# Performance work log

Hardware: AMD Instinct MI355X
Metric: run time of the kernel (lower is better)

Reference implementation:

```python
import jax, jax.numpy as jnp
import numpy as np

B, S, DIN, DOUT = 4, 4096, 4096, 4096
W_SCALE = 0.02  # kaiming-ish scale; keeps values inside fp8 range


def setup_inputs() -> dict:
    key = jax.random.key(0)
    k1, k2, k3 = jax.random.split(key, 3)
    x = jax.random.normal(k1, (B, S, DIN), dtype=jnp.float16)
    weight = (jax.random.normal(k2, (DOUT, DIN), dtype=jnp.float32) * W_SCALE).astype(jnp.float16)
    bias = (jax.random.normal(k3, (DOUT,), dtype=jnp.float32) * W_SCALE).astype(jnp.float16)
    return {"x": x, "weight": weight, "bias": bias}


def reference(x, weight, bias):
    # Emulate torch._scaled_mm: activations quantized to fp8 e5m2,
    # weight (transposed) quantized to fp8 e4m3fn, scale_a = scale_b = 1.0,
    # accumulate in fp32, add fp16 bias, output fp16.
    out_shape = x.shape[:-1] + (weight.shape[0],)
    x8 = x.reshape(-1, x.shape[-1]).astype(jnp.float8_e5m2)       # [M, DIN]
    w8 = weight.T.astype(jnp.float8_e4m3fn)                        # [DIN, DOUT]
    scale = jnp.float32(1.0)  # scale_a * scale_b
    acc = jnp.matmul(x8.astype(jnp.float32), w8.astype(jnp.float32))  # [M, DOUT] fp32 accum
    out = (acc * scale + bias.astype(jnp.float32)).astype(jnp.float16)
    return out.reshape(out_shape)
```

## Files before the change

### kernel.cpp

```cpp
#include <hip/hip_runtime.h>
#include <hip/hip_fp16.h>

#define M_DIM 16384
#define N_DIM 4096
#define K_DIM 4096

typedef __attribute__((ext_vector_type(16))) float f32x16;
typedef __attribute__((ext_vector_type(4)))  int   i32x4;
typedef __attribute__((ext_vector_type(8)))  int   i32x8;

union frag_u { i32x8 v; i32x4 h[2]; };

template<bool E4M3>
__global__ __launch_bounds__(256) void quant_tile_kernel(
    const float* __restrict__ in,
    uint4* __restrict__ out,
    int ngrp)
{
  int t = blockIdx.x * 256 + threadIdx.x;
  if (t >= ngrp) return;
  const int g    = t & 1023;
  const int tile = t >> 10;
  const int kt   = tile & 63;
  const int bt   = tile >> 6;
  const int sb   = g >> 7;
  const int half = (g >> 6) & 1;
  const int l    = g & 63;
  const int row  = bt * 256 + sb * 32 + (l & 31);
  const int k    = kt * 64 + (l >> 5) * 32 + half * 16;

  const float4* p = reinterpret_cast<const float4*>(in + (size_t)row * K_DIM + k);
  float4 v0 = p[0], v1 = p[1], v2 = p[2], v3 = p[3];
  int w0 = 0, w1 = 0, w2 = 0, w3 = 0;
  if (E4M3) {
    w0 = __builtin_amdgcn_cvt_pk_fp8_f32(v0.x, v0.y, w0, false);
    w0 = __builtin_amdgcn_cvt_pk_fp8_f32(v0.z, v0.w, w0, true);
    w1 = __builtin_amdgcn_cvt_pk_fp8_f32(v1.x, v1.y, w1, false);
    w1 = __builtin_amdgcn_cvt_pk_fp8_f32(v1.z, v1.w, w1, true);
    w2 = __builtin_amdgcn_cvt_pk_fp8_f32(v2.x, v2.y, w2, false);
    w2 = __builtin_amdgcn_cvt_pk_fp8_f32(v2.z, v2.w, w2, true);
    w3 = __builtin_amdgcn_cvt_pk_fp8_f32(v3.x, v3.y, w3, false);
    w3 = __builtin_amdgcn_cvt_pk_fp8_f32(v3.z, v3.w, w3, true);
  } else {
    w0 = __builtin_amdgcn_cvt_pk_bf8_f32(v0.x, v0.y, w0, false);
    w0 = __builtin_amdgcn_cvt_pk_bf8_f32(v0.z, v0.w, w0, true);
    w1 = __builtin_amdgcn_cvt_pk_bf8_f32(v1.x, v1.y, w1, false);
    w1 = __builtin_amdgcn_cvt_pk_bf8_f32(v1.z, v1.w, w1, true);
    w2 = __builtin_amdgcn_cvt_pk_bf8_f32(v2.x, v2.y, w2, false);
    w2 = __builtin_amdgcn_cvt_pk_bf8_f32(v2.z, v2.w, w2, true);
    w3 = __builtin_amdgcn_cvt_pk_bf8_f32(v3.x, v3.y, w3, false);
    w3 = __builtin_amdgcn_cvt_pk_bf8_f32(v3.z, v3.w, w3, true);
  }
  out[t] = make_uint4((unsigned)w0, (unsigned)w1, (unsigned)w2, (unsigned)w3);
}

__global__ __launch_bounds__(512, 2) void gemm_fp8_kernel(
    const unsigned char* __restrict__ Aq,
    const unsigned char* __restrict__ Wq,
    const float* __restrict__ bias,
    float* __restrict__ C)
{
  __shared__ __align__(16) unsigned char lds[131072];

  const int tid  = threadIdx.x;
  const int lane = tid & 63;
  const int wave = tid >> 6;
  const int wr   = wave >> 2;
  const int wc   = wave & 3;

  const int bid = blockIdx.x;
  const int swz = (bid & 7) * 128 + (bid >> 3);
  const int bmi = swz >> 4;
  const int bni = swz & 15;

  const unsigned char* tA = Aq + (size_t)bmi * (64 * 16384);
  const unsigned char* tB = Wq + (size_t)bni * (64 * 16384);

  const size_t t16 = (size_t)tid * 16;
  const int    w1k = wave * 1024;

#define STAGE(gb, lo_)                                                      \
  __builtin_amdgcn_global_load_lds(                                        \
      (const __attribute__((address_space(1))) void*)((gb) + t16),          \
      (__attribute__((address_space(3))) void*)(lds + (lo_) + w1k), 16, 0, 0)

#define STAGE_TILE(tp, base)                                                \
  STAGE(tA + (tp), (base));          STAGE(tA + (tp) + 8192, (base) + 8192); \
  STAGE(tB + (tp), (base) + 16384);  STAGE(tB + (tp) + 8192, (base) + 24576)

#define RD8(dst, off)                                                       \
  { const unsigned char* _p = lds + (off) + lane * 16;                      \
    (dst).h[0] = *reinterpret_cast<const i32x4*>(_p);                       \
    (dst).h[1] = *reinterpret_cast<const i32x4*>(_p + 1024); }

#define MFMA(d, a, b)                                                       \
  d = __builtin_amdgcn_mfma_scale_f32_32x32x64_f8f6f4(                      \
      a, b, d, 1 , 0 , 0, 0x7F7F7F7F, 0, 0x7F7F7F7F)

#define SBAR __builtin_amdgcn_sched_barrier(0)
#define P1   __builtin_amdgcn_s_setprio(1)
#define P0   __builtin_amdgcn_s_setprio(0)

  const int aoff = wr * 8192;
  const int boff = 16384 + wc * 4096;

  f32x16 acc[4][2] = {};
  frag_u Ea0, Ea1, Ea2, Ea3, Eb0, Eb1;
  frag_u Oa0, Oa1, Oa2, Oa3, Ob0, Ob1;

#define RDTILE(s, buf)                                                      \
  RD8(s##a0, (buf) + aoff);        RD8(s##a1, (buf) + aoff + 2048);         \
  RD8(s##a2, (buf) + aoff + 4096); RD8(s##a3, (buf) + aoff + 6144);         \
  RD8(s##b0, (buf) + boff);        RD8(s##b1, (buf) + boff + 2048)

#define TILE_STEP(rdset, mfset, rdbuf, stbuf, tp3)                          \
  SBAR;                                                                     \
  RDTILE(rdset, rdbuf);                                                     \
  SBAR;                                                                     \
  P1;                                                                       \
  MFMA(acc[0][0], mfset##a0.v, mfset##b0.v);                                \
  MFMA(acc[0][1], mfset##a0.v, mfset##b1.v);                                \
  MFMA(acc[1][0], mfset##a1.v, mfset##b0.v);                                \
  MFMA(acc[1][1], mfset##a1.v, mfset##b1.v);                                \
  MFMA(acc[2][0], mfset##a2.v, mfset##b0.v);                                \
  MFMA(acc[2][1], mfset##a2.v, mfset##b1.v);                                \
  MFMA(acc[3][0], mfset##a3.v, mfset##b0.v);                                \
  MFMA(acc[3][1], mfset##a3.v, mfset##b1.v);                                \
  P0;                                                                       \
  SBAR;                                                                     \
  STAGE_TILE(tp3, stbuf);                                                   \
  SBAR;                                                                     \
  asm volatile("s_waitcnt vmcnt(4)" ::: "memory");                          \
  SBAR;                                                                     \
  __builtin_amdgcn_s_barrier()

  STAGE_TILE(0, 0);
  STAGE_TILE(16384, 32768);
  STAGE_TILE(32768, 65536);
  SBAR;
  asm volatile("s_waitcnt vmcnt(4)" ::: "memory");
  SBAR;
  __builtin_amdgcn_s_barrier();
  SBAR;
  RDTILE(E, 0);
  SBAR;

  for (int it = 0; it < 16; ++it) {
    const int t = it << 2;
    const size_t tp3 = (size_t)((t + 3) & 63) * 16384;
    const size_t tp4 = (size_t)((t + 4) & 63) * 16384;
    const size_t tp5 = (size_t)((t + 5) & 63) * 16384;
    const size_t tp6 = (size_t)((t + 6) & 63) * 16384;
    TILE_STEP(O, E, 32768, 98304, tp3);
    TILE_STEP(E, O, 65536, 0, tp4);
    TILE_STEP(O, E, 98304, 32768, tp5);
    TILE_STEP(E, O, 0, 65536, tp6);
  }
#undef STAGE
#undef STAGE_TILE
#undef RD8
#undef RDTILE
#undef MFMA
#undef TILE_STEP
#undef SBAR
#undef P1
#undef P0

  #pragma unroll
  for (int n = 0; n < 2; ++n) {
    const int col = bni * 256 + wc * 64 + n * 32 + (lane & 31);
    const float bv = bias[col];
    #pragma unroll
    for (int m = 0; m < 4; ++m) {
      const int rbase = bmi * 256 + wr * 128 + m * 32 + ((lane >> 5) << 2);
      #pragma unroll
      for (int r = 0; r < 16; ++r) {
        const int row = rbase + (r & 3) + 8 * (r >> 2);
        C[(size_t)row * N_DIM + col] =
            __half2float(__float2half_rn(acc[m][n][r] + bv));
      }
    }
  }
}

extern "C" void kernel_launch(void* const* d_in, const int* in_sizes, int n_in,
                              void* d_out, int out_size, void* d_ws, size_t ws_size,
                              hipStream_t stream) {
  const float* x  = (const float*)d_in[0];
  const float* w  = (const float*)d_in[1];
  const float* bs = (const float*)d_in[2];
  float* out = (float*)d_out;

  unsigned char* xq = (unsigned char*)d_ws;
  unsigned char* wq = (unsigned char*)d_ws + (size_t)M_DIM * K_DIM;

  const int ngx = (M_DIM * K_DIM) / 16;
  const int ngw = (N_DIM * K_DIM) / 16;
  quant_tile_kernel<false><<<ngx / 256, 256, 0, stream>>>(x, (uint4*)xq, ngx);
  quant_tile_kernel<true ><<<ngw / 256, 256, 0, stream>>>(w, (uint4*)wq, ngw);

  gemm_fp8_kernel<<<1024, 512, 0, stream>>>(xq, wq, bs, out);
}
```

Before: 352.9 us.

## Stagger MFMA/LDS-read order across wave rows and fuse quantization launches

Waves in the upper row keep reading LDS fragments before issuing MFMAs, while waves in the lower row issue MFMAs first and then read, so LDS reads and matrix ops from different waves overlap more instead of contending in lockstep. Separately, the two fp8 quantization kernels (x to e5m2, weight to e4m3) are merged into one launch that picks its input by block index. This removes one kernel launch and its tail but makes the format choice a runtime branch. The per-wave ordering split risks register pressure and only pays off if the scheduler actually interleaves the two groups.

```diff
diff --git a/kernel.cpp b/kernel.cpp
--- a/kernel.cpp
+++ b/kernel.cpp
@@ -11,14 +11,18 @@
 
 union frag_u { i32x8 v; i32x4 h[2]; };
 
-template<bool E4M3>
-__global__ __launch_bounds__(256) void quant_tile_kernel(
-    const float* __restrict__ in,
-    uint4* __restrict__ out,
-    int ngrp)
+__global__ __launch_bounds__(256) void quant_fused_kernel(
+    const float* __restrict__ x, const float* __restrict__ w,
+    uint4* __restrict__ xq, uint4* __restrict__ wq)
 {
-  int t = blockIdx.x * 256 + threadIdx.x;
-  if (t >= ngrp) return;
+  const int b = blockIdx.x;
+  const float* in;
+  uint4* out;
+  int t;
+  bool e4m3;
+  if (b < 16384) { in = x; out = xq; t = b * 256 + threadIdx.x; e4m3 = false; }
+  else { in = w; out = wq; t = (b - 16384) * 256 + threadIdx.x; e4m3 = true; }
+
   const int g    = t & 1023;
   const int tile = t >> 10;
   const int kt   = tile & 63;
@@ -32,7 +36,7 @@
   const float4* p = reinterpret_cast<const float4*>(in + (size_t)row * K_DIM + k);
   float4 v0 = p[0], v1 = p[1], v2 = p[2], v3 = p[3];
   int w0 = 0, w1 = 0, w2 = 0, w3 = 0;
-  if (E4M3) {
+  if (e4m3) {
     w0 = __builtin_amdgcn_cvt_pk_fp8_f32(v0.x, v0.y, w0, false);
     w0 = __builtin_amdgcn_cvt_pk_fp8_f32(v0.z, v0.w, w0, true);
     w1 = __builtin_amdgcn_cvt_pk_fp8_f32(v1.x, v1.y, w1, false);
@@ -113,27 +117,27 @@
   RD8(s##a2, (buf) + aoff + 4096); RD8(s##a3, (buf) + aoff + 6144);         \
   RD8(s##b0, (buf) + boff);        RD8(s##b1, (buf) + boff + 2048)
 
-#define TILE_STEP(rdset, mfset, rdbuf, stbuf, tp3)                          \
+#define MFMAC(s)                                                            \
+  P1;                                                                       \
+  MFMA(acc[0][0], s##a0.v, s##b0.v);  MFMA(acc[0][1], s##a0.v, s##b1.v);    \
+  MFMA(acc[1][0], s##a1.v, s##b0.v);  MFMA(acc[1][1], s##a1.v, s##b1.v);    \
+  MFMA(acc[2][0], s##a2.v, s##b0.v);  MFMA(acc[2][1], s##a2.v, s##b1.v);    \
+  MFMA(acc[3][0], s##a3.v, s##b0.v);  MFMA(acc[3][1], s##a3.v, s##b1.v);    \
+  P0
+
+#define TAIL(stbuf, tp)                                                     \
   SBAR;                                                                     \
-  RDTILE(rdset, rdbuf);                                                     \
-  SBAR;                                                                     \
-  P1;                                                                       \
-  MFMA(acc[0][0], mfset##a0.v, mfset##b0.v);                                \
-  MFMA(acc[0][1], mfset##a0.v, mfset##b1.v);                                \
-  MFMA(acc[1][0], mfset##a1.v, mfset##b0.v);                                \
-  MFMA(acc[1][1], mfset##a1.v, mfset##b1.v);                                \
-  MFMA(acc[2][0], mfset##a2.v, mfset##b0.v);                                \
-  MFMA(acc[2][1], mfset##a2.v, mfset##b1.v);                                \
-  MFMA(acc[3][0], mfset##a3.v, mfset##b0.v);                                \
-  MFMA(acc[3][1], mfset##a3.v, mfset##b1.v);                                \
-  P0;                                                                       \
-  SBAR;                                                                     \
-  STAGE_TILE(tp3, stbuf);                                                   \
+  STAGE_TILE(tp, stbuf);                                                    \
   SBAR;                                                                     \
   asm volatile("s_waitcnt vmcnt(4)" ::: "memory");                          \
   SBAR;                                                                     \
   __builtin_amdgcn_s_barrier()
 
+#define TILE_RF(rdset, mfset, rdbuf, stbuf, tp)                             \
+  SBAR; RDTILE(rdset, rdbuf); SBAR; MFMAC(mfset); TAIL(stbuf, tp)
+#define TILE_FR(rdset, mfset, rdbuf, stbuf, tp)                             \
+  SBAR; MFMAC(mfset); SBAR; RDTILE(rdset, rdbuf); TAIL(stbuf, tp)
+
   STAGE_TILE(0, 0);
   STAGE_TILE(16384, 32768);
   STAGE_TILE(32768, 65536);
@@ -145,23 +149,40 @@
   RDTILE(E, 0);
   SBAR;
 
-  for (int it = 0; it < 16; ++it) {
-    const int t = it << 2;
-    const size_t tp3 = (size_t)((t + 3) & 63) * 16384;
-    const size_t tp4 = (size_t)((t + 4) & 63) * 16384;
-    const size_t tp5 = (size_t)((t + 5) & 63) * 16384;
-    const size_t tp6 = (size_t)((t + 6) & 63) * 16384;
-    TILE_STEP(O, E, 32768, 98304, tp3);
-    TILE_STEP(E, O, 65536, 0, tp4);
-    TILE_STEP(O, E, 98304, 32768, tp5);
-    TILE_STEP(E, O, 0, 65536, tp6);
+  if (wr == 0) {
+    for (int it = 0; it < 16; ++it) {
+      const int t = it << 2;
+      const size_t tp3 = (size_t)((t + 3) & 63) * 16384;
+      const size_t tp4 = (size_t)((t + 4) & 63) * 16384;
+      const size_t tp5 = (size_t)((t + 5) & 63) * 16384;
+      const size_t tp6 = (size_t)((t + 6) & 63) * 16384;
+      TILE_RF(O, E, 32768, 98304, tp3);
+      TILE_RF(E, O, 65536, 0,     tp4);
+      TILE_RF(O, E, 98304, 32768, tp5);
+      TILE_RF(E, O, 0,     65536, tp6);
+    }
+  } else {
+    for (int it = 0; it < 16; ++it) {
+      const int t = it << 2;
+      const size_t tp3 = (size_t)((t + 3) & 63) * 16384;
+      const size_t tp4 = (size_t)((t + 4) & 63) * 16384;
+      const size_t tp5 = (size_t)((t + 5) & 63) * 16384;
+      const size_t tp6 = (size_t)((t + 6) & 63) * 16384;
+      TILE_FR(O, E, 32768, 98304, tp3);
+      TILE_FR(E, O, 65536, 0,     tp4);
+      TILE_FR(O, E, 98304, 32768, tp5);
+      TILE_FR(E, O, 0,     65536, tp6);
+    }
   }
 #undef STAGE
 #undef STAGE_TILE
 #undef RD8
 #undef RDTILE
 #undef MFMA
-#undef TILE_STEP
+#undef MFMAC
+#undef TAIL
+#undef TILE_RF
+#undef TILE_FR
 #undef SBAR
 #undef P1
 #undef P0
@@ -194,10 +215,7 @@
   unsigned char* xq = (unsigned char*)d_ws;
   unsigned char* wq = (unsigned char*)d_ws + (size_t)M_DIM * K_DIM;
 
-  const int ngx = (M_DIM * K_DIM) / 16;
-  const int ngw = (N_DIM * K_DIM) / 16;
-  quant_tile_kernel<false><<<ngx / 256, 256, 0, stream>>>(x, (uint4*)xq, ngx);
-  quant_tile_kernel<true ><<<ngw / 256, 256, 0, stream>>>(w, (uint4*)wq, ngw);
+  quant_fused_kernel<<<20480, 256, 0, stream>>>(x, w, (uint4*)xq, (uint4*)wq);
 
   gemm_fp8_kernel<<<1024, 512, 0, stream>>>(xq, wq, bs, out);
 }
```

Result: no change. 347.7 us (-1.5%).
